# Kernel optimization log

Hardware: AMD Instinct MI355X
Metric: run time of the kernel (lower is better)

Reference implementation:

```python
import jax, jax.numpy as jnp
import numpy as np

L = 4        # num decoder layers
H = 8        # heads
D = 512      # d_model
DFF = 2048   # ffn hidden
V = 8000     # target vocab
B = 16       # batch
S_ENC = 128  # encoder seq len
T = 32       # decode target_length
START, END, NULL = 1, 2, 0
NEG = -1e9
EPS = 1e-6


def sinusoid_pos(max_len, d):
    pos = np.arange(max_len)[:, None].astype(np.float32)
    i = np.arange(d)[None, :].astype(np.float32)
    ang = pos / np.power(10000.0, (2.0 * np.floor(i / 2.0)) / d)
    pe = np.where(np.arange(d)[None, :] % 2 == 0, np.sin(ang), np.cos(ang))
    return jnp.asarray(pe[None], jnp.float32)  # [1, max_len, d]


def setup_inputs() -> dict:
    key = jax.random.key(0)
    ks = jax.random.split(key, 16)
    g = lambda k, shape: jax.random.normal(k, shape, jnp.float32) * 0.02
    return {
        "target_length": T,
        "encoder_output": jax.random.normal(ks[0], (B, S_ENC, D), jnp.float32),
        "padding_mask": jnp.zeros((B, S_ENC), jnp.float32),  # 1.0 where padded
        "embed": g(ks[1], (V, D)),
        "wq": g(ks[2], (L, D, D)), "wk": g(ks[3], (L, D, D)),
        "wv": g(ks[4], (L, D, D)), "wo": g(ks[5], (L, D, D)),
        "cwq": g(ks[6], (L, D, D)), "cwk": g(ks[7], (L, D, D)),
        "cwv": g(ks[8], (L, D, D)), "cwo": g(ks[9], (L, D, D)),
        "w1": g(ks[10], (L, D, DFF)), "b1": jnp.zeros((L, DFF), jnp.float32),
        "w2": g(ks[11], (L, DFF, D)), "b2": jnp.zeros((L, D), jnp.float32),
        "ln_g": jnp.ones((L, 3, D), jnp.float32), "ln_b": jnp.zeros((L, 3, D), jnp.float32),
        "fc_w": g(ks[12], (D, V)), "fc_b": jnp.zeros((V,), jnp.float32),
    }


def ln(x, g, b):
    m = jnp.mean(x, axis=-1, keepdims=True)
    v = jnp.mean(jnp.square(x - m), axis=-1, keepdims=True)
    return (x - m) * jax.lax.rsqrt(v + EPS) * g + b


def mha(q_in, kv_in, wq, wk, wv, wo, mask):
    Bn, Sq, d = q_in.shape
    dh = d // H
    q = (q_in @ wq).reshape(Bn, Sq, H, dh)
    k = (kv_in @ wk).reshape(Bn, -1, H, dh)
    v = (kv_in @ wv).reshape(Bn, -1, H, dh)
    s = jnp.einsum('bqhd,bkhd->bhqk', q, k) / jnp.sqrt(jnp.float32(dh)) + mask
    a = jax.nn.softmax(s, axis=-1)
    o = jnp.einsum('bhqk,bkhd->bqhd', a, v).reshape(Bn, Sq, d)
    return o @ wo


def decoder_stack(x, encoder_output, self_mask, cross_mask,
                  wq, wk, wv, wo, cwq, cwk, cwv, cwo,
                  w1, b1, w2, b2, ln_g, ln_b):
    for i in range(L):
        a = mha(x, x, wq[i], wk[i], wv[i], wo[i], self_mask)
        x = ln(x + a, ln_g[i, 0], ln_b[i, 0])
        a2 = mha(x, encoder_output, cwq[i], cwk[i], cwv[i], cwo[i], cross_mask)
        x = ln(x + a2, ln_g[i, 1], ln_b[i, 1])
        f = jax.nn.relu(x @ w1[i] + b1[i]) @ w2[i] + b2[i]
        x = ln(x + f, ln_g[i, 2], ln_b[i, 2])
    return x


def reference(target_length, encoder_output, padding_mask, embed,
              wq, wk, wv, wo, cwq, cwk, cwv, cwo,
              w1, b1, w2, b2, ln_g, ln_b, fc_w, fc_b):
    Bn, S, d = encoder_output.shape
    Tp1 = target_length + 1
    pos_enc = sinusoid_pos(Tp1, d)
    sqrt_d = jnp.sqrt(jnp.float32(d))
    cross_mask = padding_mask[:, None, None, :] * NEG  # [B,1,1,S_enc]
    tokens0 = jnp.full((Bn, Tp1), NULL, jnp.int32).at[:, 0].set(START)
    done0 = jnp.zeros((Bn,), bool)

    def step(carry, t):
        tokens, done = carry
        # re-embed the whole (fixed-size, masked) prefix buffer each step
        x = embed[tokens] * sqrt_d + pos_enc
        # only positions <= t are valid keys; no look-ahead mask (matches original)
        self_mask = jnp.where(jnp.arange(Tp1) <= t, 0.0, NEG)[None, None, None, :]
        x = decoder_stack(x, encoder_output, self_mask, cross_mask,
                          wq, wk, wv, wo, cwq, cwk, cwv, cwo,
                          w1, b1, w2, b2, ln_g, ln_b)
        out = x[:, t, :] @ fc_w + fc_b  # logits at last valid position
        max_idx = jnp.argmax(out, axis=-1).astype(jnp.int32)
        done = done | (max_idx == END)
        tok = jnp.where(done, jnp.int32(NULL), max_idx)
        tokens = tokens.at[:, t + 1].set(tok)
        return (tokens, done), None

    (tokens, done), _ = jax.lax.scan(step, (tokens0, done0), jnp.arange(target_length))
    return tokens[:, 1:].astype(jnp.int64)
```

## Files before the change

### kernel.cpp

```cpp
#include <hip/hip_runtime.h>
#include <math.h>

#define L_   4
#define H_   8
#define D_   512
#define DH   64
#define DFF_ 2048
#define V_   8000
#define B_   16
#define SENC 128
#define T_   32
#define TP1  33
#define NEGV -1e9f
#define EPSV 1e-6f
#define SQRTD 22.627416997969522f
#define XSZ  ((size_t)TP1 * B_ * D_)

__global__ __launch_bounds__(256) void gemm32_k(
    const float* __restrict__ A, const float* __restrict__ W,
    const float* __restrict__ bias, float* __restrict__ C,
    int M, int N, int K, int kchunk, size_t pstride, int relu, int tmode)
{
    __shared__ __align__(16) float As[2][16][68];
    __shared__ __align__(16) float Bs[2][16][68];
    int tid = threadIdx.x;
    int tx = tid & 15, ty = tid >> 4;
    int m0 = blockIdx.y * 64, n0 = blockIdx.x * 64;
    int kbeg = blockIdx.z * kchunk;
    int niter = kchunk >> 4;
    C += (size_t)blockIdx.z * pstride;
    int am = tid >> 2, aseg = tid & 3;
    int bk = tid >> 4, bc4 = (tid & 15) * 4;
    float4 aReg = make_float4(0.f, 0.f, 0.f, 0.f), bReg;
    {
        int gm = m0 + am;
        if (gm < M) aReg = *(const float4*)&A[(size_t)gm * K + kbeg + aseg * 4];
        bReg = *(const float4*)&W[(size_t)(kbeg + bk) * N + n0 + bc4];
    }
    As[0][aseg * 4 + 0][am] = aReg.x;
    As[0][aseg * 4 + 1][am] = aReg.y;
    As[0][aseg * 4 + 2][am] = aReg.z;
    As[0][aseg * 4 + 3][am] = aReg.w;
    *(float4*)&Bs[0][bk][bc4] = bReg;
    __syncthreads();
    float acc[4][4] = {};
    for (int it = 0; it < niter; it++) {
        int cur = it & 1;
        if (it + 1 < niter) {
            int k0 = kbeg + (it + 1) * 16;
            int gm = m0 + am;
            aReg = make_float4(0.f, 0.f, 0.f, 0.f);
            if (gm < M) aReg = *(const float4*)&A[(size_t)gm * K + k0 + aseg * 4];
            bReg = *(const float4*)&W[(size_t)(k0 + bk) * N + n0 + bc4];
        }
        #pragma unroll
        for (int kk = 0; kk < 16; kk++) {
            float4 a4 = *(const float4*)&As[cur][kk][ty * 4];
            float4 b4 = *(const float4*)&Bs[cur][kk][tx * 4];
            acc[0][0] += a4.x * b4.x; acc[0][1] += a4.x * b4.y;
            acc[0][2] += a4.x * b4.z; acc[0][3] += a4.x * b4.w;
            acc[1][0] += a4.y * b4.x; acc[1][1] += a4.y * b4.y;
            acc[1][2] += a4.y * b4.z; acc[1][3] += a4.y * b4.w;
            acc[2][0] += a4.z * b4.x; acc[2][1] += a4.z * b4.y;
            acc[2][2] += a4.z * b4.z; acc[2][3] += a4.z * b4.w;
            acc[3][0] += a4.w * b4.x; acc[3][1] += a4.w * b4.y;
            acc[3][2] += a4.w * b4.z; acc[3][3] += a4.w * b4.w;
        }
        if (it + 1 < niter) {
            int nxt = 1 - cur;
            As[nxt][aseg * 4 + 0][am] = aReg.x;
            As[nxt][aseg * 4 + 1][am] = aReg.y;
            As[nxt][aseg * 4 + 2][am] = aReg.z;
            As[nxt][aseg * 4 + 3][am] = aReg.w;
            *(float4*)&Bs[nxt][bk][bc4] = bReg;
        }
        __syncthreads();
    }
    #pragma unroll
    for (int i = 0; i < 4; i++) {
        int gm = m0 + ty * 4 + i;
        if (gm >= M) continue;
        if (tmode == 1) {
            #pragma unroll
            for (int j = 0; j < 4; j++) {
                int gn = n0 + tx * 4 + j;
                float vv = acc[i][j];
                if (bias) vv += bias[gn];
                if (relu) vv = fmaxf(vv, 0.f);
                C[(size_t)(gm >> 7) * 65536 + (size_t)gn * SENC + (gm & 127)] = vv;
            }
        } else {
            int gn = n0 + tx * 4;
            float4 o;
            o.x = acc[i][0]; o.y = acc[i][1]; o.z = acc[i][2]; o.w = acc[i][3];
            if (bias) {
                o.x += bias[gn + 0]; o.y += bias[gn + 1];
                o.z += bias[gn + 2]; o.w += bias[gn + 3];
            }
            if (relu) {
                o.x = fmaxf(o.x, 0.f); o.y = fmaxf(o.y, 0.f);
                o.z = fmaxf(o.z, 0.f); o.w = fmaxf(o.w, 0.f);
            }
            *(float4*)&C[(size_t)gm * N + gn] = o;
        }
    }
}

__global__ __launch_bounds__(256) void gemm_qkv_k(
    const float* __restrict__ A, const float* __restrict__ W0,
    const float* __restrict__ W1, const float* __restrict__ W2,
    float* __restrict__ Cb, int M)
{
    __shared__ __align__(16) float As[2][16][68];
    __shared__ __align__(16) float Bs[2][16][68];
    int sel = blockIdx.x >> 3;
    const float* W = (sel == 0) ? W0 : ((sel == 1) ? W1 : W2);
    float* C = Cb + (size_t)sel * XSZ;
    int tid = threadIdx.x;
    int tx = tid & 15, ty = tid >> 4;
    int m0 = blockIdx.y * 64, n0 = (blockIdx.x & 7) * 64;
    int am = tid >> 2, aseg = tid & 3;
    int bk = tid >> 4, bc4 = (tid & 15) * 4;
    float4 aReg = make_float4(0.f, 0.f, 0.f, 0.f), bReg;
    {
        int gm = m0 + am;
        if (gm < M) aReg = *(const float4*)&A[(size_t)gm * D_ + aseg * 4];
        bReg = *(const float4*)&W[(size_t)bk * D_ + n0 + bc4];
    }
    As[0][aseg * 4 + 0][am] = aReg.x;
    As[0][aseg * 4 + 1][am] = aReg.y;
    As[0][aseg * 4 + 2][am] = aReg.z;
    As[0][aseg * 4 + 3][am] = aReg.w;
    *(float4*)&Bs[0][bk][bc4] = bReg;
    __syncthreads();
    float acc[4][4] = {};
    for (int it = 0; it < 32; it++) {
        int cur = it & 1;
        if (it + 1 < 32) {
            int k0 = (it + 1) * 16;
            int gm = m0 + am;
            aReg = make_float4(0.f, 0.f, 0.f, 0.f);
            if (gm < M) aReg = *(const float4*)&A[(size_t)gm * D_ + k0 + aseg * 4];
            bReg = *(const float4*)&W[(size_t)(k0 + bk) * D_ + n0 + bc4];
        }
        #pragma unroll
        for (int kk = 0; kk < 16; kk++) {
            float4 a4 = *(const float4*)&As[cur][kk][ty * 4];
            float4 b4 = *(const float4*)&Bs[cur][kk][tx * 4];
            acc[0][0] += a4.x * b4.x; acc[0][1] += a4.x * b4.y;
            acc[0][2] += a4.x * b4.z; acc[0][3] += a4.x * b4.w;
            acc[1][0] += a4.y * b4.x; acc[1][1] += a4.y * b4.y;
            acc[1][2] += a4.y * b4.z; acc[1][3] += a4.y * b4.w;
            acc[2][0] += a4.z * b4.x; acc[2][1] += a4.z * b4.y;
            acc[2][2] += a4.z * b4.z; acc[2][3] += a4.z * b4.w;
            acc[3][0] += a4.w * b4.x; acc[3][1] += a4.w * b4.y;
            acc[3][2] += a4.w * b4.z; acc[3][3] += a4.w * b4.w;
        }
        if (it + 1 < 32) {
            int nxt = 1 - cur;
            As[nxt][aseg * 4 + 0][am] = aReg.x;
            As[nxt][aseg * 4 + 1][am] = aReg.y;
            As[nxt][aseg * 4 + 2][am] = aReg.z;
            As[nxt][aseg * 4 + 3][am] = aReg.w;
            *(float4*)&Bs[nxt][bk][bc4] = bReg;
        }
        __syncthreads();
    }
    #pragma unroll
    for (int i = 0; i < 4; i++) {
        int gm = m0 + ty * 4 + i;
        if (gm >= M) continue;
        if (sel == 1) {
            #pragma unroll
            for (int j = 0; j < 4; j++) {
                int gn = n0 + tx * 4 + j;
                C[(size_t)(gm & 15) * 16896 + (size_t)gn * TP1 + (gm >> 4)] =
                    acc[i][j];
            }
        } else {
            float4 o;
            o.x = acc[i][0]; o.y = acc[i][1]; o.z = acc[i][2]; o.w = acc[i][3];
            *(float4*)&C[(size_t)gm * D_ + n0 + tx * 4] = o;
        }
    }
}

__global__ void init_k(int* __restrict__ tokens, int* __restrict__ done,
                       float* __restrict__ cmask, const float* __restrict__ pm)
{
    int tid = threadIdx.x + blockIdx.x * 256;
    if (tid < B_ * TP1) tokens[tid] = ((tid % TP1) == 0) ? 1 : 0;
    if (tid < B_) done[tid] = 0;
    if (tid < B_ * SENC) cmask[tid] = pm[tid] * NEGV;
}

__global__ __launch_bounds__(256) void embed_k(
    const float* __restrict__ embed, const int* __restrict__ tokens,
    float* __restrict__ x)
{
    int p = blockIdx.x;
    int b = blockIdx.y;
    int tok = tokens[b * TP1 + p];
    const float* e = embed + (size_t)tok * D_;
    float* xr = x + ((size_t)p * B_ + b) * D_;
    for (int d = threadIdx.x; d < D_; d += 256) {
        float fd = (float)(2 * (d / 2)) / (float)D_;
        float ang = (float)p / powf(10000.f, fd);
        float pe = (d & 1) ? cosf(ang) : sinf(ang);
        xr[d] = e[d] * SQRTD + pe;
    }
}

__device__ __forceinline__ float block_sum(float s) {
    __shared__ float red[4];
    #pragma unroll
    for (int off = 32; off; off >>= 1) s += __shfl_xor(s, off);
    if ((threadIdx.x & 63) == 0) red[threadIdx.x >> 6] = s;
    __syncthreads();
    float tot = red[0] + red[1] + red[2] + red[3];
    __syncthreads();
    return tot;
}

__device__ __forceinline__ float4 block_sum4(float4 s) {
    __shared__ __align__(16) float red4[4][4];
    #pragma unroll
    for (int off = 32; off; off >>= 1) {
        s.x += __shfl_xor(s.x, off);
        s.y += __shfl_xor(s.y, off);
        s.z += __shfl_xor(s.z, off);
        s.w += __shfl_xor(s.w, off);
    }
    if ((threadIdx.x & 63) == 0) *(float4*)red4[threadIdx.x >> 6] = s;
    __syncthreads();
    float4 t;
    t.x = red4[0][0] + red4[1][0] + red4[2][0] + red4[3][0];
    t.y = red4[0][1] + red4[1][1] + red4[2][1] + red4[3][1];
    t.z = red4[0][2] + red4[1][2] + red4[2][2] + red4[3][2];
    t.w = red4[0][3] + red4[1][3] + red4[2][3] + red4[3][3];
    __syncthreads();
    return t;
}

__global__ __launch_bounds__(256) void attn_mega_k(
    const float* __restrict__ q, const float* __restrict__ kT,
    const float* __restrict__ v, const float* __restrict__ wo,
    const float* __restrict__ KcT, const float* __restrict__ Vc,
    const float* __restrict__ cmask, const float* __restrict__ cwq,
    const float* __restrict__ cwo, float* __restrict__ x,
    const float* __restrict__ lg, const float* __restrict__ lb, int P)
{
    int b = blockIdx.x;
    int p0 = blockIdx.y * 4;
    int tid = threadIdx.x;
    int c0 = tid * 2;
    __shared__ float xs[4][D_];
    __shared__ float arow[4][D_];
    __shared__ float scs[4][H_][SENC + 4];
    __shared__ float inv[4][H_];
    #pragma unroll
    for (int g = 0; g < 4; g++) {
        float2 qv = make_float2(0.f, 0.f);
        if (p0 + g < P)
            qv = *(const float2*)&q[((size_t)(p0 + g) * B_ + b) * D_ + c0];
        *(float2*)&arow[g][c0] = qv;
    }
    __syncthreads();
    {
        int h = tid >> 5, kp = tid & 31;
        float a0 = 0.f, a1 = 0.f, a2 = 0.f, a3 = 0.f;
        if (kp < P) {
            const float* kb = kT + ((size_t)(b * 8 + h) * 64) * TP1 + kp;
            #pragma unroll 8
            for (int d = 0; d < 64; d++) {
                float kv = kb[(size_t)d * TP1];
                a0 += arow[0][h * 64 + d] * kv;
                a1 += arow[1][h * 64 + d] * kv;
                a2 += arow[2][h * 64 + d] * kv;
                a3 += arow[3][h * 64 + d] * kv;
            }
        }
        scs[0][h][kp] = a0 * 0.125f;
        scs[1][h][kp] = a1 * 0.125f;
        scs[2][h][kp] = a2 * 0.125f;
        scs[3][h][kp] = a3 * 0.125f;
    }
    __syncthreads();
    {
        int gh = tid >> 3, lane8 = tid & 7;
        int g = gh >> 3, h = gh & 7;
        float mx = -1e30f;
        for (int j = lane8; j < P; j += 8) mx = fmaxf(mx, scs[g][h][j]);
        mx = fmaxf(mx, __shfl_xor(mx, 1));
        mx = fmaxf(mx, __shfl_xor(mx, 2));
        mx = fmaxf(mx, __shfl_xor(mx, 4));
        float sum = 0.f;
        for (int j = lane8; j < P; j += 8) {
            float e = expf(scs[g][h][j] - mx);
            scs[g][h][j] = e;
            sum += e;
        }
        sum += __shfl_xor(sum, 1);
        sum += __shfl_xor(sum, 2);
        sum += __shfl_xor(sum, 4);
        if (lane8 == 0) inv[g][h] = 1.f / sum;
    }
    __syncthreads();
    {
        int h = tid >> 5;
        float o0[4] = {0.f, 0.f, 0.f, 0.f}, o1[4] = {0.f, 0.f, 0.f, 0.f};
        for (int j = 0; j < P; j++) {
            float2 vv = *(const float2*)&v[((size_t)j * B_ + b) * D_ + c0];
            #pragma unroll
            for (int g = 0; g < 4; g++) {
                float w = scs[g][h][j];
                o0[g] += w * vv.x; o1[g] += w * vv.y;
            }
        }
        #pragma unroll
        for (int g = 0; g < 4; g++) {
            arow[g][c0]     = o0[g] * inv[g][h];
            arow[g][c0 + 1] = o1[g] * inv[g][h];
        }
    }
    __syncthreads();
    {
        float v0[4], v1[4];
        #pragma unroll
        for (int g = 0; g < 4; g++) {
            float2 xv = make_float2(0.f, 0.f);
            if (p0 + g < P)
                xv = *(const float2*)&x[((size_t)(p0 + g) * B_ + b) * D_ + c0];
            v0[g] = xv.x; v1[g] = xv.y;
        }
        #pragma unroll 8
        for (int k = 0; k < D_; k++) {
            float2 wv = *(const float2*)&wo[(size_t)k * D_ + c0];
            #pragma unroll
            for (int g = 0; g < 4; g++) {
                float a = arow[g][k];
                v0[g] += a * wv.x; v1[g] += a * wv.y;
            }
        }
        float4 s1 = make_float4(v0[0] + v1[0], v0[1] + v1[1],
                                v0[2] + v1[2], v0[3] + v1[3]);
        float4 m4 = block_sum4(s1);
        float mean[4] = {m4.x * (1.f / 512.f), m4.y * (1.f / 512.f),
                         m4.z * (1.f / 512.f), m4.w * (1.f / 512.f)};
        float d0[4], d1[4];
        #pragma unroll
        for (int g = 0; g < 4; g++) {
            d0[g] = v0[g] - mean[g]; d1[g] = v1[g] - mean[g];
        }
        float4 s2 = make_float4(d0[0] * d0[0] + d1[0] * d1[0],
                                d0[1] * d0[1] + d1[1] * d1[1],
                                d0[2] * d0[2] + d1[2] * d1[2],
                                d0[3] * d0[3] + d1[3] * d1[3]);
        float4 w4 = block_sum4(s2);
        float var[4] = {w4.x * (1.f / 512.f), w4.y * (1.f / 512.f),
                        w4.z * (1.f / 512.f), w4.w * (1.f / 512.f)};
        float g0 = lg[c0], g1 = lg[c0 + 1];
        float bb0 = lb[c0], bb1 = lb[c0 + 1];
        #pragma unroll
        for (int g = 0; g < 4; g++) {
            float rs = rsqrtf(var[g] + EPSV);
            xs[g][c0]     = d0[g] * rs * g0 + bb0;
            xs[g][c0 + 1] = d1[g] * rs * g1 + bb1;
        }
    }
    __syncthreads();
    {
        float q0[4] = {0.f, 0.f, 0.f, 0.f}, q1[4] = {0.f, 0.f, 0.f, 0.f};
        #pragma unroll 8
        for (int k = 0; k < D_; k++) {
            float2 wv = *(const float2*)&cwq[(size_t)k * D_ + c0];
            #pragma unroll
            for (int g = 0; g < 4; g++) {
                float a = xs[g][k];
                q0[g] += a * wv.x; q1[g] += a * wv.y;
            }
        }
        #pragma unroll
        for (int g = 0; g < 4; g++) {
            arow[g][c0] = q0[g]; arow[g][c0 + 1] = q1[g];
        }
    }
    __syncthreads();
    #pragma unroll
    for (int i = 0; i < 4; i++) {
        int idx = tid + i * 256;
        int h = idx >> 7, s = idx & 127;
        const float* kb = KcT + ((size_t)(b * 512 + h * 64)) * SENC + s;
        float a0 = 0.f, a1 = 0.f, a2 = 0.f, a3 = 0.f;
        #pragma unroll 8
        for (int d = 0; d < 64; d++) {
            float kc = kb[(size_t)d * SENC];
            a0 += arow[0][h * 64 + d] * kc;
            a1 += arow[1][h * 64 + d] * kc;
            a2 += arow[2][h * 64 + d] * kc;
            a3 += arow[3][h * 64 + d] * kc;
        }
        float cm = cmask[b * SENC + s];
        scs[0][h][s] = a0 * 0.125f + cm;
        scs[1][h][s] = a1 * 0.125f + cm;
        scs[2][h][s] = a2 * 0.125f + cm;
        scs[3][h][s] = a3 * 0.125f + cm;
    }
    __syncthreads();
    {
        int gh = tid >> 3, lane8 = tid & 7;
        int g = gh >> 3, h = gh & 7;
        float mx = -1e30f;
        for (int s = lane8; s < SENC; s += 8) mx = fmaxf(mx, scs[g][h][s]);
        mx = fmaxf(mx, __shfl_xor(mx, 1));
        mx = fmaxf(mx, __shfl_xor(mx, 2));
        mx = fmaxf(mx, __shfl_xor(mx, 4));
        float sum = 0.f;
        for (int s = lane8; s < SENC; s += 8) {
            float e = expf(scs[g][h][s] - mx);
            scs[g][h][s] = e;
            sum += e;
        }
        sum += __shfl_xor(sum, 1);
        sum += __shfl_xor(sum, 2);
        sum += __shfl_xor(sum, 4);
        if (lane8 == 0) inv[g][h] = 1.f / sum;
    }
    __syncthreads();
    {
        int h = tid >> 5;
        float o0[4] = {0.f, 0.f, 0.f, 0.f}, o1[4] = {0.f, 0.f, 0.f, 0.f};
        for (int s = 0; s < SENC; s++) {
            float2 vv = *(const float2*)&Vc[((size_t)b * SENC + s) * D_ + c0];
            #pragma unroll
            for (int g = 0; g < 4; g++) {
                float w = scs[g][h][s];
                o0[g] += w * vv.x; o1[g] += w * vv.y;
            }
        }
        #pragma unroll
        for (int g = 0; g < 4; g++) {
            arow[g][c0]     = o0[g] * inv[g][h];
            arow[g][c0 + 1] = o1[g] * inv[g][h];
        }
    }
    __syncthreads();
    {
        float v0[4], v1[4];
        #pragma unroll
        for (int g = 0; g < 4; g++) {
            v0[g] = xs[g][c0]; v1[g] = xs[g][c0 + 1];
        }
        #pragma unroll 8
        for (int k = 0; k < D_; k++) {
            float2 wv = *(const float2*)&cwo[(size_t)k * D_ + c0];
            #pragma unroll
            for (int g = 0; g < 4; g++) {
                float a = arow[g][k];
                v0[g] += a * wv.x; v1[g] += a * wv.y;
            }
        }
        float4 s1 = make_float4(v0[0] + v1[0], v0[1] + v1[1],
                                v0[2] + v1[2], v0[3] + v1[3]);
        float4 m4 = block_sum4(s1);
        float mean[4] = {m4.x * (1.f / 512.f), m4.y * (1.f / 512.f),
                         m4.z * (1.f / 512.f), m4.w * (1.f / 512.f)};
        float d0[4], d1[4];
        #pragma unroll
        for (int g = 0; g < 4; g++) {
            d0[g] = v0[g] - mean[g]; d1[g] = v1[g] - mean[g];
        }
        float4 s2 = make_float4(d0[0] * d0[0] + d1[0] * d1[0],
                                d0[1] * d0[1] + d1[1] * d1[1],
                                d0[2] * d0[2] + d1[2] * d1[2],
                                d0[3] * d0[3] + d1[3] * d1[3]);
        float4 w4 = block_sum4(s2);
        float var[4] = {w4.x * (1.f / 512.f), w4.y * (1.f / 512.f),
                        w4.z * (1.f / 512.f), w4.w * (1.f / 512.f)};
        float g0 = lg[D_ + c0], g1 = lg[D_ + c0 + 1];
        float bb0 = lb[D_ + c0], bb1 = lb[D_ + c0 + 1];
        #pragma unroll
        for (int g = 0; g < 4; g++) {
            if (p0 + g < P) {
                float rs = rsqrtf(var[g] + EPSV);
                float* xr = x + ((size_t)(p0 + g) * B_ + b) * D_;
                xr[c0]     = d0[g] * rs * g0 + bb0;
                xr[c0 + 1] = d1[g] * rs * g1 + bb1;
            }
        }
    }
}

__global__ __launch_bounds__(256) void ln_red_k(
    float* __restrict__ x, const float* __restrict__ parts, size_t pstride,
    int nparts, const float* __restrict__ bias,
    const float* __restrict__ gam, const float* __restrict__ bet)
{
    int r = blockIdx.x;
    float* xr = x + (size_t)r * D_;
    int tid = threadIdx.x;
    float v0 = xr[tid];
    float v1 = xr[tid + 256];
    for (int s = 0; s < nparts; s++) {
        const float* pr = parts + (size_t)s * pstride + (size_t)r * D_;
        v0 += pr[tid];
        v1 += pr[tid + 256];
    }
    if (bias) { v0 += bias[tid]; v1 += bias[tid + 256]; }
    float mean = block_sum(v0 + v1) * (1.f / 512.f);
    float d0 = v0 - mean, d1 = v1 - mean;
    float var = block_sum(d0 * d0 + d1 * d1) * (1.f / 512.f);
    float rs = rsqrtf(var + EPSV);
    xr[tid]       = d0 * rs * gam[tid] + bet[tid];
    xr[tid + 256] = d1 * rs * gam[tid + 256] + bet[tid + 256];
}

__global__ __launch_bounds__(256) void logits_k(
    const float* __restrict__ x, const float* __restrict__ fcw,
    const float* __restrict__ fcb, float* __restrict__ cand_v,
    int* __restrict__ cand_i, int t)
{
    __shared__ float xs[B_][D_];
    __shared__ float red[4][64][B_];
    int tid = threadIdx.x;
    for (int i = tid; i < B_ * D_; i += 256) {
        int b = i >> 9, d = i & 511;
        xs[b][d] = x[((size_t)t * B_ + b) * D_ + d];
    }
    __syncthreads();
    int lane = tid & 63, ks = tid >> 6;
    int col = blockIdx.x * 64 + lane;
    float acc[B_] = {};
    int kb = ks * 128;
    for (int k = kb; k < kb + 128; k++) {
        float w = fcw[(size_t)k * V_ + col];
        #pragma unroll
        for (int b = 0; b < B_; b++) acc[b] += xs[b][k] * w;
    }
    #pragma unroll
    for (int b = 0; b < B_; b++) red[ks][lane][b] = acc[b];
    __syncthreads();
    if (ks == 0) {
        float bias = fcb[col];
        #pragma unroll
        for (int b = 0; b < B_; b++) {
            float val = red[0][lane][b] + red[1][lane][b]
                      + red[2][lane][b] + red[3][lane][b] + bias;
            int idx = col;
            #pragma unroll
            for (int off = 32; off; off >>= 1) {
                float ov = __shfl_down(val, off);
                int oi = __shfl_down(idx, off);
                if (ov > val || (ov == val && oi < idx)) { val = ov; idx = oi; }
            }
            if (lane == 0) {
                cand_v[(size_t)b * 125 + blockIdx.x] = val;
                cand_i[(size_t)b * 125 + blockIdx.x] = idx;
            }
        }
    }
}

__global__ __launch_bounds__(128) void argmax_k(
    const float* __restrict__ cand_v, const int* __restrict__ cand_i,
    int* __restrict__ tokens, int* __restrict__ done, int t)
{
    int b = blockIdx.x;
    int tid = threadIdx.x;
    float val = -1e30f; int idx = 0x7fffffff;
    if (tid < 125) { val = cand_v[(size_t)b * 125 + tid]; idx = cand_i[(size_t)b * 125 + tid]; }
    __shared__ float sv[128];
    __shared__ int si[128];
    sv[tid] = val; si[tid] = idx;
    __syncthreads();
    for (int s = 64; s; s >>= 1) {
        if (tid < s) {
            float ov = sv[tid + s]; int oi = si[tid + s];
            if (ov > sv[tid] || (ov == sv[tid] && oi < si[tid])) {
                sv[tid] = ov; si[tid] = oi;
            }
        }
        __syncthreads();
    }
    if (tid == 0) {
        int best = si[0];
        int dn = done[b] | (best == 2 ? 1 : 0);
        done[b] = dn;
        tokens[b * TP1 + t + 1] = dn ? 0 : best;
    }
}

__global__ void writeout_k(const int* __restrict__ tokens, int* __restrict__ out)
{
    int i = threadIdx.x + blockIdx.x * 256;
    if (i < B_ * T_) {
        int b = i / T_, j = i % T_;
        out[i] = tokens[b * TP1 + j + 1];
    }
}

extern "C" void kernel_launch(void* const* d_in, const int* in_sizes, int n_in,
                              void* d_out, int out_size, void* d_ws, size_t ws_size,
                              hipStream_t stream)
{
    const float* enc   = (const float*)d_in[1];
    const float* pm    = (const float*)d_in[2];
    const float* embed = (const float*)d_in[3];
    const float* wq    = (const float*)d_in[4];
    const float* wk    = (const float*)d_in[5];
    const float* wv    = (const float*)d_in[6];
    const float* wo    = (const float*)d_in[7];
    const float* cwq   = (const float*)d_in[8];
    const float* cwk   = (const float*)d_in[9];
    const float* cwv   = (const float*)d_in[10];
    const float* cwo   = (const float*)d_in[11];
    const float* w1    = (const float*)d_in[12];
    const float* b1    = (const float*)d_in[13];
    const float* w2    = (const float*)d_in[14];
    const float* b2    = (const float*)d_in[15];
    const float* ln_g  = (const float*)d_in[16];
    const float* ln_b  = (const float*)d_in[17];
    const float* fcw   = (const float*)d_in[18];
    const float* fcb   = (const float*)d_in[19];

    float* ws = (float*)d_ws;
    size_t off = 0;
    float* x     = ws + off; off += XSZ;
    float* qkv   = ws + off; off += 3 * XSZ;
    float* parts = ws + off; off += 4 * XSZ;
    float* ffnh  = ws + off; off += (size_t)TP1 * B_ * DFF_;
    float* cand_v= ws + off; off += (size_t)B_ * 125;
    float* KcT   = ws + off; off += (size_t)L_ * B_ * SENC * D_;
    float* Vc    = ws + off; off += (size_t)L_ * B_ * SENC * D_;
    float* cmask = ws + off; off += (size_t)B_ * SENC;
    int* cand_i  = (int*)(ws + off); off += (size_t)B_ * 125;
    int* tokens  = (int*)(ws + off); off += (B_ * TP1 + 63) & ~63;
    int* done    = (int*)(ws + off); off += 64;

    init_k<<<8, 256, 0, stream>>>(tokens, done, cmask, pm);

    const size_t KVL = (size_t)B_ * SENC * D_;
    for (int l = 0; l < L_; l++) {
        gemm32_k<<<dim3(8, (B_ * SENC) / 64), 256, 0, stream>>>(
            enc, cwk + (size_t)l * D_ * D_, nullptr, KcT + l * KVL,
            B_ * SENC, D_, D_, D_, 0, 0, 1);
        gemm32_k<<<dim3(8, (B_ * SENC) / 64), 256, 0, stream>>>(
            enc, cwv + (size_t)l * D_ * D_, nullptr, Vc + l * KVL,
            B_ * SENC, D_, D_, D_, 0, 0, 0);
    }

    for (int t = 0; t < T_; t++) {
        int P = t + 1;
        int M = P * B_;
        int mt = (M + 63) / 64;

        embed_k<<<dim3(P, B_), 256, 0, stream>>>(embed, tokens, x);

        for (int l = 0; l < L_; l++) {
            const size_t lw = (size_t)l * D_ * D_;
            gemm_qkv_k<<<dim3(24, mt), 256, 0, stream>>>(
                x, wq + lw, wk + lw, wv + lw, qkv, M);
            attn_mega_k<<<dim3(B_, (P + 3) / 4), 256, 0, stream>>>(
                qkv, qkv + XSZ, qkv + 2 * XSZ, wo + lw,
                KcT + l * KVL, Vc + l * KVL, cmask, cwq + lw, cwo + lw, x,
                ln_g + (size_t)(l * 3 + 0) * D_, ln_b + (size_t)(l * 3 + 0) * D_, P);
            gemm32_k<<<dim3(32, mt), 256, 0, stream>>>(
                x, w1 + (size_t)l * D_ * DFF_, b1 + (size_t)l * DFF_, ffnh,
                M, DFF_, D_, D_, 0, 1, 0);
            gemm32_k<<<dim3(8, mt, 4), 256, 0, stream>>>(
                ffnh, w2 + (size_t)l * DFF_ * D_, nullptr, parts,
                M, D_, DFF_, 512, XSZ, 0, 0);
            ln_red_k<<<M, 256, 0, stream>>>(x, parts, XSZ, 4, b2 + (size_t)l * D_,
                ln_g + (size_t)(l * 3 + 2) * D_, ln_b + (size_t)(l * 3 + 2) * D_);
        }

        logits_k<<<V_ / 64, 256, 0, stream>>>(x, fcw, fcb, cand_v, cand_i, t);
        argmax_k<<<B_, 128, 0, stream>>>(cand_v, cand_i, tokens, done, t);
    }

    writeout_k<<<2, 256, 0, stream>>>(tokens, (int*)d_out);
}
```

Baseline: 25.52 ms.

## Halve GEMM M-tile, fuse argmax into embed, precompute positional encoding

The GEMM kernels now use 32-row M tiles with 2x4 per-thread outputs, which doubles the block count for the small decode-step matrices so more CUs are busy. The per-step argmax kernel is folded into the next step's embedding kernel and the final argmax into writeout, removing one launch per step. The positional encoding is computed once into a table instead of calling powf/sin/cos every step. Costs are more redundant B-tile loads per output, idle threads during A loads, and scalar stores replacing the float4 stores.

```diff
diff --git a/kernel.cpp b/kernel.cpp
--- a/kernel.cpp
+++ b/kernel.cpp
@@ -21,11 +21,11 @@
     const float* __restrict__ bias, float* __restrict__ C,
     int M, int N, int K, int kchunk, size_t pstride, int relu, int tmode)
 {
-    __shared__ __align__(16) float As[2][16][68];
+    __shared__ __align__(16) float As[2][16][34];
     __shared__ __align__(16) float Bs[2][16][68];
     int tid = threadIdx.x;
     int tx = tid & 15, ty = tid >> 4;
-    int m0 = blockIdx.y * 64, n0 = blockIdx.x * 64;
+    int m0 = blockIdx.y * 32, n0 = blockIdx.x * 64;
     int kbeg = blockIdx.z * kchunk;
     int niter = kchunk >> 4;
     C += (size_t)blockIdx.z * pstride;
@@ -33,75 +33,68 @@
     int bk = tid >> 4, bc4 = (tid & 15) * 4;
     float4 aReg = make_float4(0.f, 0.f, 0.f, 0.f), bReg;
     {
-        int gm = m0 + am;
-        if (gm < M) aReg = *(const float4*)&A[(size_t)gm * K + kbeg + aseg * 4];
-        bReg = *(const float4*)&W[(size_t)(kbeg + bk) * N + n0 + bc4];
-    }
-    As[0][aseg * 4 + 0][am] = aReg.x;
-    As[0][aseg * 4 + 1][am] = aReg.y;
-    As[0][aseg * 4 + 2][am] = aReg.z;
-    As[0][aseg * 4 + 3][am] = aReg.w;
+        int k0 = kbeg;
+        if (tid < 128) {
+            int gm = m0 + am;
+            if (gm < M) aReg = *(const float4*)&A[(size_t)gm * K + k0 + aseg * 4];
+        }
+        bReg = *(const float4*)&W[(size_t)(k0 + bk) * N + n0 + bc4];
+    }
+    if (tid < 128) {
+        As[0][aseg * 4 + 0][am] = aReg.x;
+        As[0][aseg * 4 + 1][am] = aReg.y;
+        As[0][aseg * 4 + 2][am] = aReg.z;
+        As[0][aseg * 4 + 3][am] = aReg.w;
+    }
     *(float4*)&Bs[0][bk][bc4] = bReg;
     __syncthreads();
-    float acc[4][4] = {};
+    float acc[2][4] = {};
     for (int it = 0; it < niter; it++) {
         int cur = it & 1;
         if (it + 1 < niter) {
             int k0 = kbeg + (it + 1) * 16;
-            int gm = m0 + am;
-            aReg = make_float4(0.f, 0.f, 0.f, 0.f);
-            if (gm < M) aReg = *(const float4*)&A[(size_t)gm * K + k0 + aseg * 4];
+            if (tid < 128) {
+                int gm = m0 + am;
+                aReg = make_float4(0.f, 0.f, 0.f, 0.f);
+                if (gm < M) aReg = *(const float4*)&A[(size_t)gm * K + k0 + aseg * 4];
+            }
             bReg = *(const float4*)&W[(size_t)(k0 + bk) * N + n0 + bc4];
         }
         #pragma unroll
         for (int kk = 0; kk < 16; kk++) {
-            float4 a4 = *(const float4*)&As[cur][kk][ty * 4];
+            float2 a2 = *(const float2*)&As[cur][kk][ty * 2];
             float4 b4 = *(const float4*)&Bs[cur][kk][tx * 4];
-            acc[0][0] += a4.x * b4.x; acc[0][1] += a4.x * b4.y;
-            acc[0][2] += a4.x * b4.z; acc[0][3] += a4.x * b4.w;
-            acc[1][0] += a4.y * b4.x; acc[1][1] += a4.y * b4.y;
-            acc[1][2] += a4.y * b4.z; acc[1][3] += a4.y * b4.w;
-            acc[2][0] += a4.z * b4.x; acc[2][1] += a4.z * b4.y;
-            acc[2][2] += a4.z * b4.z; acc[2][3] += a4.z * b4.w;
-            acc[3][0] += a4.w * b4.x; acc[3][1] += a4.w * b4.y;
-            acc[3][2] += a4.w * b4.z; acc[3][3] += a4.w * b4.w;
+            acc[0][0] += a2.x * b4.x; acc[0][1] += a2.x * b4.y;
+            acc[0][2] += a2.x * b4.z; acc[0][3] += a2.x * b4.w;
+            acc[1][0] += a2.y * b4.x; acc[1][1] += a2.y * b4.y;
+            acc[1][2] += a2.y * b4.z; acc[1][3] += a2.y * b4.w;
         }
         if (it + 1 < niter) {
             int nxt = 1 - cur;
-            As[nxt][aseg * 4 + 0][am] = aReg.x;
-            As[nxt][aseg * 4 + 1][am] = aReg.y;
-            As[nxt][aseg * 4 + 2][am] = aReg.z;
-            As[nxt][aseg * 4 + 3][am] = aReg.w;
+            if (tid < 128) {
+                As[nxt][aseg * 4 + 0][am] = aReg.x;
+                As[nxt][aseg * 4 + 1][am] = aReg.y;
+                As[nxt][aseg * 4 + 2][am] = aReg.z;
+                As[nxt][aseg * 4 + 3][am] = aReg.w;
+            }
             *(float4*)&Bs[nxt][bk][bc4] = bReg;
         }
         __syncthreads();
     }
     #pragma unroll
-    for (int i = 0; i < 4; i++) {
-        int gm = m0 + ty * 4 + i;
+    for (int i = 0; i < 2; i++) {
+        int gm = m0 + ty * 2 + i;
         if (gm >= M) continue;
-        if (tmode == 1) {
-            #pragma unroll
-            for (int j = 0; j < 4; j++) {
-                int gn = n0 + tx * 4 + j;
-                float vv = acc[i][j];
-                if (bias) vv += bias[gn];
-                if (relu) vv = fmaxf(vv, 0.f);
+        #pragma unroll
+        for (int j = 0; j < 4; j++) {
+            int gn = n0 + tx * 4 + j;
+            float vv = acc[i][j];
+            if (bias) vv += bias[gn];
+            if (relu) vv = fmaxf(vv, 0.f);
+            if (tmode == 1)
                 C[(size_t)(gm >> 7) * 65536 + (size_t)gn * SENC + (gm & 127)] = vv;
-            }
-        } else {
-            int gn = n0 + tx * 4;
-            float4 o;
-            o.x = acc[i][0]; o.y = acc[i][1]; o.z = acc[i][2]; o.w = acc[i][3];
-            if (bias) {
-                o.x += bias[gn + 0]; o.y += bias[gn + 1];
-                o.z += bias[gn + 2]; o.w += bias[gn + 3];
-            }
-            if (relu) {
-                o.x = fmaxf(o.x, 0.f); o.y = fmaxf(o.y, 0.f);
-                o.z = fmaxf(o.z, 0.f); o.w = fmaxf(o.w, 0.f);
-            }
-            *(float4*)&C[(size_t)gm * N + gn] = o;
+            else
+                C[(size_t)gm * N + gn] = vv;
         }
     }
 }
@@ -111,76 +104,77 @@
     const float* __restrict__ W1, const float* __restrict__ W2,
     float* __restrict__ Cb, int M)
 {
-    __shared__ __align__(16) float As[2][16][68];
+    __shared__ __align__(16) float As[2][16][34];
     __shared__ __align__(16) float Bs[2][16][68];
     int sel = blockIdx.x >> 3;
     const float* W = (sel == 0) ? W0 : ((sel == 1) ? W1 : W2);
     float* C = Cb + (size_t)sel * XSZ;
     int tid = threadIdx.x;
     int tx = tid & 15, ty = tid >> 4;
-    int m0 = blockIdx.y * 64, n0 = (blockIdx.x & 7) * 64;
+    int m0 = blockIdx.y * 32, n0 = (blockIdx.x & 7) * 64;
     int am = tid >> 2, aseg = tid & 3;
     int bk = tid >> 4, bc4 = (tid & 15) * 4;
     float4 aReg = make_float4(0.f, 0.f, 0.f, 0.f), bReg;
     {
-        int gm = m0 + am;
-        if (gm < M) aReg = *(const float4*)&A[(size_t)gm * D_ + aseg * 4];
+        if (tid < 128) {
+            int gm = m0 + am;
+            if (gm < M) aReg = *(const float4*)&A[(size_t)gm * D_ + aseg * 4];
+        }
         bReg = *(const float4*)&W[(size_t)bk * D_ + n0 + bc4];
     }
-    As[0][aseg * 4 + 0][am] = aReg.x;
-    As[0][aseg * 4 + 1][am] = aReg.y;
-    As[0][aseg * 4 + 2][am] = aReg.z;
-    As[0][aseg * 4 + 3][am] = aReg.w;
+    if (tid < 128) {
+        As[0][aseg * 4 + 0][am] = aReg.x;
+        As[0][aseg * 4 + 1][am] = aReg.y;
+        As[0][aseg * 4 + 2][am] = aReg.z;
+        As[0][aseg * 4 + 3][am] = aReg.w;
+    }
     *(float4*)&Bs[0][bk][bc4] = bReg;
     __syncthreads();
-    float acc[4][4] = {};
+    float acc[2][4] = {};
     for (int it = 0; it < 32; it++) {
         int cur = it & 1;
         if (it + 1 < 32) {
             int k0 = (it + 1) * 16;
-            int gm = m0 + am;
-            aReg = make_float4(0.f, 0.f, 0.f, 0.f);
-            if (gm < M) aReg = *(const float4*)&A[(size_t)gm * D_ + k0 + aseg * 4];
+            if (tid < 128) {
+                int gm = m0 + am;
+                aReg = make_float4(0.f, 0.f, 0.f, 0.f);
+                if (gm < M) aReg = *(const float4*)&A[(size_t)gm * D_ + k0 + aseg * 4];
+            }
             bReg = *(const float4*)&W[(size_t)(k0 + bk) * D_ + n0 + bc4];
         }
         #pragma unroll
         for (int kk = 0; kk < 16; kk++) {
-            float4 a4 = *(const float4*)&As[cur][kk][ty * 4];
+            float2 a2 = *(const float2*)&As[cur][kk][ty * 2];
             float4 b4 = *(const float4*)&Bs[cur][kk][tx * 4];
-            acc[0][0] += a4.x * b4.x; acc[0][1] += a4.x * b4.y;
-            acc[0][2] += a4.x * b4.z; acc[0][3] += a4.x * b4.w;
-            acc[1][0] += a4.y * b4.x; acc[1][1] += a4.y * b4.y;
-            acc[1][2] += a4.y * b4.z; acc[1][3] += a4.y * b4.w;
-            acc[2][0] += a4.z * b4.x; acc[2][1] += a4.z * b4.y;
-            acc[2][2] += a4.z * b4.z; acc[2][3] += a4.z * b4.w;
-            acc[3][0] += a4.w * b4.x; acc[3][1] += a4.w * b4.y;
-            acc[3][2] += a4.w * b4.z; acc[3][3] += a4.w * b4.w;
+            acc[0][0] += a2.x * b4.x; acc[0][1] += a2.x * b4.y;
+            acc[0][2] += a2.x * b4.z; acc[0][3] += a2.x * b4.w;
+            acc[1][0] += a2.y * b4.x; acc[1][1] += a2.y * b4.y;
+            acc[1][2] += a2.y * b4.z; acc[1][3] += a2.y * b4.w;
         }
         if (it + 1 < 32) {
             int nxt = 1 - cur;
-            As[nxt][aseg * 4 + 0][am] = aReg.x;
-            As[nxt][aseg * 4 + 1][am] = aReg.y;
-            As[nxt][aseg * 4 + 2][am] = aReg.z;
-            As[nxt][aseg * 4 + 3][am] = aReg.w;
+            if (tid < 128) {
+                As[nxt][aseg * 4 + 0][am] = aReg.x;
+                As[nxt][aseg * 4 + 1][am] = aReg.y;
+                As[nxt][aseg * 4 + 2][am] = aReg.z;
+                As[nxt][aseg * 4 + 3][am] = aReg.w;
+            }
             *(float4*)&Bs[nxt][bk][bc4] = bReg;
         }
         __syncthreads();
     }
     #pragma unroll
-    for (int i = 0; i < 4; i++) {
-        int gm = m0 + ty * 4 + i;
+    for (int i = 0; i < 2; i++) {
+        int gm = m0 + ty * 2 + i;
         if (gm >= M) continue;
-        if (sel == 1) {
-            #pragma unroll
-            for (int j = 0; j < 4; j++) {
-                int gn = n0 + tx * 4 + j;
+        #pragma unroll
+        for (int j = 0; j < 4; j++) {
+            int gn = n0 + tx * 4 + j;
+            if (sel == 1)
                 C[(size_t)(gm & 15) * 16896 + (size_t)gn * TP1 + (gm >> 4)] =
                     acc[i][j];
-            }
-        } else {
-            float4 o;
-            o.x = acc[i][0]; o.y = acc[i][1]; o.z = acc[i][2]; o.w = acc[i][3];
-            *(float4*)&C[(size_t)gm * D_ + n0 + tx * 4] = o;
+            else
+                C[(size_t)gm * D_ + gn] = acc[i][j];
         }
     }
 }
@@ -194,21 +188,68 @@
     if (tid < B_ * SENC) cmask[tid] = pm[tid] * NEGV;
 }
 
-__global__ __launch_bounds__(256) void embed_k(
-    const float* __restrict__ embed, const int* __restrict__ tokens,
-    float* __restrict__ x)
+__global__ __launch_bounds__(256) void pe_k(float* __restrict__ pe)
 {
     int p = blockIdx.x;
-    int b = blockIdx.y;
-    int tok = tokens[b * TP1 + p];
-    const float* e = embed + (size_t)tok * D_;
-    float* xr = x + ((size_t)p * B_ + b) * D_;
     for (int d = threadIdx.x; d < D_; d += 256) {
         float fd = (float)(2 * (d / 2)) / (float)D_;
         float ang = (float)p / powf(10000.f, fd);
-        float pe = (d & 1) ? cosf(ang) : sinf(ang);
-        xr[d] = e[d] * SQRTD + pe;
-    }
+        pe[(size_t)p * D_ + d] = (d & 1) ? cosf(ang) : sinf(ang);
+    }
+}
+
+__global__ __launch_bounds__(256) void embed_k(
+    const float* __restrict__ embed, int* __restrict__ tokens,
+    float* __restrict__ x, const float* __restrict__ pe,
+    const float* __restrict__ cand_v, const int* __restrict__ cand_i,
+    int* __restrict__ done, int t)
+{
+    int p = blockIdx.x;
+    int b = blockIdx.y;
+    int tid = threadIdx.x;
+    __shared__ float sv[128];
+    __shared__ int si[128];
+    __shared__ int stok;
+    if (p == t && t > 0) {
+        if (tid < 128) {
+            float val = -1e30f; int idx = 0x7fffffff;
+            if (tid < 125) {
+                val = cand_v[(size_t)b * 125 + tid];
+                idx = cand_i[(size_t)b * 125 + tid];
+            }
+            sv[tid] = val; si[tid] = idx;
+        }
+        __syncthreads();
+        for (int s = 64; s; s >>= 1) {
+            if (tid < s) {
+                float ov = sv[tid + s]; int oi = si[tid + s];
+                if (ov > sv[tid] || (ov == sv[tid] && oi < si[tid])) {
+                    sv[tid] = ov; si[tid] = oi;
+                }
+            }
+            __syncthreads();
+        }
+        if (tid == 0) {
+            int best = si[0];
+            int dn = done[b] | (best == 2 ? 1 : 0);
+            done[b] = dn;
+            int tk = dn ? 0 : best;
+            tokens[b * TP1 + t] = tk;
+            stok = tk;
+        }
+        __syncthreads();
+    }
+    int tok = (p == t && t > 0) ? stok : tokens[b * TP1 + p];
+    const float* e = embed + (size_t)tok * D_;
+    const float* pr = pe + (size_t)p * D_;
+    float* xr = x + ((size_t)p * B_ + b) * D_;
+    int c0 = tid * 2;
+    float2 ev = *(const float2*)&e[c0];
+    float2 pv = *(const float2*)&pr[c0];
+    float2 o;
+    o.x = ev.x * SQRTD + pv.x;
+    o.y = ev.y * SQRTD + pv.y;
+    *(float2*)&xr[c0] = o;
 }
 
 __device__ __forceinline__ float block_sum(float s) {
@@ -561,16 +602,21 @@
     }
 }
 
-__global__ __launch_bounds__(128) void argmax_k(
-    const float* __restrict__ cand_v, const int* __restrict__ cand_i,
-    int* __restrict__ tokens, int* __restrict__ done, int t)
+__global__ __launch_bounds__(128) void writeout_k(
+    const int* __restrict__ tokens, const float* __restrict__ cand_v,
+    const int* __restrict__ cand_i, const int* __restrict__ done,
+    int* __restrict__ out)
 {
     int b = blockIdx.x;
     int tid = threadIdx.x;
-    float val = -1e30f; int idx = 0x7fffffff;
-    if (tid < 125) { val = cand_v[(size_t)b * 125 + tid]; idx = cand_i[(size_t)b * 125 + tid]; }
     __shared__ float sv[128];
     __shared__ int si[128];
+    __shared__ int stok;
+    float val = -1e30f; int idx = 0x7fffffff;
+    if (tid < 125) {
+        val = cand_v[(size_t)b * 125 + tid];
+        idx = cand_i[(size_t)b * 125 + tid];
+    }
     sv[tid] = val; si[tid] = idx;
     __syncthreads();
     for (int s = 64; s; s >>= 1) {
@@ -585,18 +631,11 @@
     if (tid == 0) {
         int best = si[0];
         int dn = done[b] | (best == 2 ? 1 : 0);
-        done[b] = dn;
-        tokens[b * TP1 + t + 1] = dn ? 0 : best;
-    }
-}
-
-__global__ void writeout_k(const int* __restrict__ tokens, int* __restrict__ out)
-{
-    int i = threadIdx.x + blockIdx.x * 256;
-    if (i < B_ * T_) {
-        int b = i / T_, j = i % T_;
-        out[i] = tokens[b * TP1 + j + 1];
-    }
+        stok = dn ? 0 : best;
+    }
+    __syncthreads();
+    if (tid < T_)
+        out[b * T_ + tid] = (tid == T_ - 1) ? stok : tokens[b * TP1 + tid + 1];
 }
 
 extern "C" void kernel_launch(void* const* d_in, const int* in_sizes, int n_in,
@@ -633,18 +672,20 @@
     float* KcT   = ws + off; off += (size_t)L_ * B_ * SENC * D_;
     float* Vc    = ws + off; off += (size_t)L_ * B_ * SENC * D_;
     float* cmask = ws + off; off += (size_t)B_ * SENC;
+    float* pe    = ws + off; off += (size_t)TP1 * D_;
     int* cand_i  = (int*)(ws + off); off += (size_t)B_ * 125;
     int* tokens  = (int*)(ws + off); off += (B_ * TP1 + 63) & ~63;
     int* done    = (int*)(ws + off); off += 64;
 
     init_k<<<8, 256, 0, stream>>>(tokens, done, cmask, pm);
+    pe_k<<<TP1, 256, 0, stream>>>(pe);
 
     const size_t KVL = (size_t)B_ * SENC * D_;
     for (int l = 0; l < L_; l++) {
-        gemm32_k<<<dim3(8, (B_ * SENC) / 64), 256, 0, stream>>>(
+        gemm32_k<<<dim3(8, (B_ * SENC) / 32), 256, 0, stream>>>(
             enc, cwk + (size_t)l * D_ * D_, nullptr, KcT + l * KVL,
             B_ * SENC, D_, D_, D_, 0, 0, 1);
-        gemm32_k<<<dim3(8, (B_ * SENC) / 64), 256, 0, stream>>>(
+        gemm32_k<<<dim3(8, (B_ * SENC) / 32), 256, 0, stream>>>(
             enc, cwv + (size_t)l * D_ * D_, nullptr, Vc + l * KVL,
             B_ * SENC, D_, D_, D_, 0, 0, 0);
     }
@@ -652,9 +693,10 @@
     for (int t = 0; t < T_; t++) {
         int P = t + 1;
         int M = P * B_;
-        int mt = (M + 63) / 64;
-
-        embed_k<<<dim3(P, B_), 256, 0, stream>>>(embed, tokens, x);
+        int mt = (M + 31) / 32;
+
+        embed_k<<<dim3(P, B_), 256, 0, stream>>>(
+            embed, tokens, x, pe, cand_v, cand_i, done, t);
 
         for (int l = 0; l < L_; l++) {
             const size_t lw = (size_t)l * D_ * D_;
@@ -675,8 +717,7 @@
         }
 
         logits_k<<<V_ / 64, 256, 0, stream>>>(x, fcw, fcb, cand_v, cand_i, t);
-        argmax_k<<<B_, 128, 0, stream>>>(cand_v, cand_i, tokens, done, t);
-    }
-
-    writeout_k<<<2, 256, 0, stream>>>(tokens, (int*)d_out);
-}
+    }
+
+    writeout_k<<<B_, 128, 0, stream>>>(tokens, cand_v, cand_i, done, (int*)d_out);
+}
```

Result: faster. 24.24 ms (-5.0%).
